# Optimization experiments

Measured on AMD Instinct MI355X. Metric: run time of the kernel, lower is better.

The kernel has to match this reference:

```python
import jax, jax.numpy as jnp
import numpy as np

N_NODES = 50000
N_EDGES = 640000
F = 128          # feat_dims == hidden_dims == out_channels
L = 5            # num_layers of GatedGraphConv


def setup_inputs() -> dict:
    key = jax.random.key(0)
    ks = jax.random.split(key, 9)
    s = 1.0 / np.sqrt(F)
    x = jax.random.normal(ks[0], (N_NODES, F), dtype=jnp.float32)
    edge_index = jax.random.randint(ks[1], (2, N_EDGES), 0, N_NODES, dtype=jnp.int64)
    weight = jax.random.uniform(ks[2], (L, F, F), jnp.float32, -s, s)   # per-layer linear
    w_ih = jax.random.uniform(ks[3], (3 * F, F), jnp.float32, -s, s)     # GRUCell input weights
    w_hh = jax.random.uniform(ks[4], (3 * F, F), jnp.float32, -s, s)     # GRUCell hidden weights
    b_ih = jax.random.uniform(ks[5], (3 * F,), jnp.float32, -s, s)
    b_hh = jax.random.uniform(ks[6], (3 * F,), jnp.float32, -s, s)
    lin_w = jax.random.uniform(ks[7], (1, F), jnp.float32, -s, s)
    lin_b = jax.random.uniform(ks[8], (1,), jnp.float32, -s, s)
    return {"x": x, "edge_index": edge_index, "weight": weight,
            "w_ih": w_ih, "w_hh": w_hh, "b_ih": b_ih, "b_hh": b_hh,
            "lin_w": lin_w, "lin_b": lin_b}


def _gru_cell(m, h, w_ih, w_hh, b_ih, b_hh):
    gi = m @ w_ih.T + b_ih          # [N, 3F]
    gh = h @ w_hh.T + b_hh          # [N, 3F]
    i_r, i_z, i_n = jnp.split(gi, 3, axis=-1)
    h_r, h_z, h_n = jnp.split(gh, 3, axis=-1)
    r = jax.nn.sigmoid(i_r + h_r)
    z = jax.nn.sigmoid(i_z + h_z)
    n = jnp.tanh(i_n + r * h_n)
    return (1.0 - z) * n + z * h


def reference(x, edge_index, weight, w_ih, w_hh, b_ih, b_hh, lin_w, lin_b):
    src = edge_index[0]   # message source (x_j)
    dst = edge_index[1]   # aggregation target
    n_nodes = x.shape[0]
    h = x  # in_channels == out_channels, no padding needed
    for i in range(L):
        m = h @ weight[i]                                   # [N, F]
        agg = jax.ops.segment_sum(m[src], dst, num_segments=n_nodes)  # add-aggregate
        h = _gru_cell(agg, h, w_ih, w_hh, b_ih, b_hh)
    out = jax.nn.relu(h) @ lin_w.T + lin_b                  # [N, 1]
    return out
```

## Files before the change

kernel.cpp:

```cpp
#include <hip/hip_runtime.h>

typedef float f32x4 __attribute__((ext_vector_type(4)));
typedef __bf16 bf16x8 __attribute__((ext_vector_type(8)));
typedef unsigned short u16x8 __attribute__((ext_vector_type(8)));

#define F 128

__device__ __forceinline__ unsigned short bf16_rne(float f) {
  unsigned u = __float_as_uint(f);
  u += 0x7FFFu + ((u >> 16) & 1u);
  return (unsigned short)(u >> 16);
}
__device__ __forceinline__ float bf16f(unsigned short s) {
  return __uint_as_float((unsigned)s << 16);
}


__global__ void split8_kernel(const float* __restrict__ in,
                              unsigned short* __restrict__ hi, unsigned short* __restrict__ lo,
                              int N) {
  int i = blockIdx.x * 256 + threadIdx.x;
  if (i >= N * 16) return;
  int node = i >> 4, f8 = i & 15;
  const float4* p = (const float4*)(in + (size_t)node * F + f8 * 8);
  float4 a = p[0], b = p[1];
  float v[8] = {a.x, a.y, a.z, a.w, b.x, b.y, b.z, b.w};
  u16x8 vh, vl;
#pragma unroll
  for (int e = 0; e < 8; ++e) {
    unsigned short x = bf16_rne(v[e]);
    vh[e] = x;
    vl[e] = bf16_rne(v[e] - bf16f(x));
  }
  size_t o = (size_t)node * F + f8 * 8;
  *(u16x8*)(hi + o) = vh;
  *(u16x8*)(lo + o) = vl;
}

__global__ void prep_w_kernel(const float* __restrict__ W, const float* __restrict__ w_ih,
                              const float* __restrict__ w_hh,
                              unsigned short* __restrict__ Bpack, int L) {
  int idx = blockIdx.x * 256 + threadIdx.x;
  if (idx >= L * 98304) return;
  int e = idx & 7;
  int l = (idx >> 3) & 63;
  int fp = idx >> 9;
  int part = fp % 3;
  int rest = fp / 3;
  int w = rest & 7, g = (rest >> 3) & 1, ks = (rest >> 4) & 3, t = rest >> 6;
  int j = part * 128 + w * 16 + (l & 15);
  int k = ks * 32 + ((l >> 4) & 3) * 8 + e;
  float v;
  if (g == 0) {
    const float* wi = w_ih + (size_t)j * 128;
    const float* wk = W + (size_t)t * 16384 + (size_t)k * 128;
    float acc = 0.f;
#pragma unroll 4
    for (int c = 0; c < 128; ++c) acc = fmaf(wk[c], wi[c], acc);
    v = acc;
  } else {
    v = w_hh[(size_t)j * 128 + k];
  }
  int ff = ((ks * 2 + g) * 8 + w) * 3 + part;
  size_t base = (size_t)t * 196608 + (size_t)ff * 1024 + l * 8 + e;
  unsigned short x = bf16_rne(v);
  Bpack[base] = x;
  Bpack[base + 512] = bf16_rne(v - bf16f(x));
}

__global__ void hist_kernel(const int* __restrict__ ei, int* __restrict__ cnt, int E) {
  int e = blockIdx.x * 256 + threadIdx.x;
  if (e < E) atomicAdd(&cnt[ei[E + e]], 1);
}

__global__ void scan1_kernel(const int* __restrict__ cnt, int* __restrict__ exscan,
                             int* __restrict__ chunk_sums, int N) {
  __shared__ int tmp[256];
  int i = blockIdx.x * 256 + threadIdx.x;
  int v = (i < N) ? cnt[i] : 0;
  tmp[threadIdx.x] = v;
  __syncthreads();
#pragma unroll
  for (int off = 1; off < 256; off <<= 1) {
    int a = (threadIdx.x >= off) ? tmp[threadIdx.x - off] : 0;
    __syncthreads();
    tmp[threadIdx.x] += a;
    __syncthreads();
  }
  if (i < N) exscan[i] = tmp[threadIdx.x] - v;
  if (threadIdx.x == 255) chunk_sums[blockIdx.x] = tmp[255];
}

__global__ void scan2_kernel(int* __restrict__ chunk_sums, int nchunk) {
  __shared__ int tmp[256];
  int v = (threadIdx.x < nchunk) ? chunk_sums[threadIdx.x] : 0;
  tmp[threadIdx.x] = v;
  __syncthreads();
#pragma unroll
  for (int off = 1; off < 256; off <<= 1) {
    int a = (threadIdx.x >= off) ? tmp[threadIdx.x - off] : 0;
    __syncthreads();
    tmp[threadIdx.x] += a;
    __syncthreads();
  }
  if (threadIdx.x < nchunk) chunk_sums[threadIdx.x] = tmp[threadIdx.x] - v;
}

__global__ void finalize_rowptr_kernel(const int* __restrict__ exscan,
                                       const int* __restrict__ chunk_sums,
                                       int* __restrict__ rowptr, int* __restrict__ cursor,
                                       int N, int E) {
  int i = blockIdx.x * 256 + threadIdx.x;
  if (i < N) {
    int v = exscan[i] + chunk_sums[i >> 8];
    rowptr[i] = v;
    cursor[i] = v;
  }
  if (i == N) rowptr[N] = E;
}

__global__ void place_kernel(const int* __restrict__ ei, int* __restrict__ cursor,
                             int* __restrict__ csr_src, int E) {
  int e = blockIdx.x * 256 + threadIdx.x;
  if (e >= E) return;
  int pos = atomicAdd(&cursor[ei[E + e]], 1);
  csr_src[pos] = ei[e];
}

__global__ __launch_bounds__(256) void gather_kernel(
    const unsigned short* __restrict__ hh, const unsigned short* __restrict__ hl,
    const int* __restrict__ rowptr, const int* __restrict__ csr_src,
    unsigned short* __restrict__ shi, unsigned short* __restrict__ slo, int N) {
  int node = blockIdx.x * 4 + (threadIdx.x >> 6);
  if (node >= N) return;
  const int lane = threadIdx.x & 63;
  const int grp = lane >> 4, sub = lane & 15;
  const int par = grp >> 1;
  const unsigned short* base = (grp & 1) ? hl : hh;
  const int beg = rowptr[node], end = rowptr[node + 1];
  float a[8] = {0.f, 0.f, 0.f, 0.f, 0.f, 0.f, 0.f, 0.f};
  int j = beg;
  for (; j + 8 <= end; j += 8) {
    int e0 = csr_src[j + par];
    int e1 = csr_src[j + 2 + par];
    int e2 = csr_src[j + 4 + par];
    int e3 = csr_src[j + 6 + par];
    u16x8 v0 = *(const u16x8*)(base + (size_t)e0 * F + sub * 8);
    u16x8 v1 = *(const u16x8*)(base + (size_t)e1 * F + sub * 8);
    u16x8 v2 = *(const u16x8*)(base + (size_t)e2 * F + sub * 8);
    u16x8 v3 = *(const u16x8*)(base + (size_t)e3 * F + sub * 8);
#pragma unroll
    for (int q = 0; q < 8; ++q)
      a[q] += (bf16f(v0[q]) + bf16f(v1[q])) + (bf16f(v2[q]) + bf16f(v3[q]));
  }
  for (; j + 2 <= end; j += 2) {
    int e0 = csr_src[j + par];
    u16x8 v0 = *(const u16x8*)(base + (size_t)e0 * F + sub * 8);
#pragma unroll
    for (int q = 0; q < 8; ++q) a[q] += bf16f(v0[q]);
  }
  if (j < end && par == 0) {
    int e0 = csr_src[j];
    u16x8 v0 = *(const u16x8*)(base + (size_t)e0 * F + sub * 8);
#pragma unroll
    for (int q = 0; q < 8; ++q) a[q] += bf16f(v0[q]);
  }
#pragma unroll
  for (int q = 0; q < 8; ++q) {
    a[q] += __shfl_xor(a[q], 32, 64);
    a[q] += __shfl_xor(a[q], 16, 64);
  }
  if (grp == 0) {
    u16x8 o;
#pragma unroll
    for (int q = 0; q < 8; ++q) o[q] = bf16_rne(a[q]);
    *(u16x8*)(shi + (size_t)node * F + sub * 8) = o;
  } else if (grp == 1) {
    u16x8 o;
#pragma unroll
    for (int q = 0; q < 8; ++q) {
      unsigned short x = bf16_rne(a[q]);
      o[q] = bf16_rne(a[q] - bf16f(x));
    }
    *(u16x8*)(slo + (size_t)node * F + sub * 8) = o;
  }
}

__device__ __forceinline__ void g2l(const void* g, void* l) {
  __builtin_amdgcn_global_load_lds((const __attribute__((address_space(1))) void*)g,
                                   (__attribute__((address_space(3))) void*)l, 16, 0, 0);
}

#define LOADB(hs, slot)                                                          \
  {                                                                              \
    const unsigned char* bg = Bbase + (size_t)(hs) * 49152;                      \
    _Pragma("unroll") for (int i = 0; i < 6; ++i)                                \
        Bf[slot][i] = *(const bf16x8*)(bg + i * 1024);                           \
  }
#define LOADA(hs, slot)                                                          \
  {                                                                              \
    const int ks_ = (hs) >> 1, g_ = (hs) & 1;                                    \
    const unsigned char* bh = lds + ((g_ * 2) * 4 + ks_) * 4096 + lrow * 64 + kq * 16;      \
    const unsigned char* bl = lds + ((g_ * 2 + 1) * 4 + ks_) * 4096 + lrow * 64 + kq * 16;  \
    _Pragma("unroll") for (int t = 0; t < 4; ++t) {                              \
      Af[slot][t] = *(const bf16x8*)(bh + t * 1024);                             \
      Af[slot][4 + t] = *(const bf16x8*)(bl + t * 1024);                         \
    }                                                                            \
  }
#define DOMFMA(hs, bslot, aslot)                                                 \
  {                                                                              \
    const int g_ = (hs) & 1;                                                     \
    __builtin_amdgcn_s_setprio(1);                                               \
    _Pragma("unroll") for (int part = 0; part < 3; ++part)                       \
        _Pragma("unroll") for (int t = 0; t < 4; ++t) {                          \
      const int ai = (part == 2) ? (t * 4 + 2 + g_) : (t * 4 + part);            \
      acc[ai] = __builtin_amdgcn_mfma_f32_16x16x32_bf16(Af[aslot][t], Bf[bslot][part * 2], acc[ai], 0, 0, 0);     \
      acc[ai] = __builtin_amdgcn_mfma_f32_16x16x32_bf16(Af[aslot][4 + t], Bf[bslot][part * 2], acc[ai], 0, 0, 0); \
      acc[ai] = __builtin_amdgcn_mfma_f32_16x16x32_bf16(Af[aslot][t], Bf[bslot][part * 2 + 1], acc[ai], 0, 0, 0); \
    }                                                                            \
    __builtin_amdgcn_s_setprio(0);                                               \
  }

#define ABSTRIDE 1056

__global__ __launch_bounds__(512, 2) void gemm_gru_kernel(
    const unsigned short* __restrict__ s_hi, const unsigned short* __restrict__ s_lo,
    const unsigned short* h_hi, const unsigned short* h_lo,
    const unsigned short* __restrict__ Bpack,
    const float* __restrict__ bih, const float* __restrict__ bhh,
    unsigned short* h_hi_out, unsigned short* h_lo_out, int N) {
  __shared__ __align__(1024) unsigned char lds[64 * ABSTRIDE];
  const int tid = threadIdx.x, w = tid >> 6, lane = tid & 63;
  const int lrow = lane & 15, kq = lane >> 4;
  const int row0 = blockIdx.x * 64;

  {
    const int arr = w >> 1;
    const unsigned short* ap = (arr == 0) ? s_hi : (arr == 1) ? s_lo : (arr == 2) ? h_hi : h_lo;
#pragma unroll
    for (int i = 0; i < 8; ++i) {
      const int ks = (2 * w + (i >> 2)) & 3;
      int r = row0 + (i & 3) * 16 + (lane >> 2);
      if (r >= N) r = N - 1;
      const unsigned short* g = ap + (size_t)r * F + ks * 32 + (lane & 3) * 8;
      g2l(g, lds + (w * 8 + i) * 1024 + lane * 16);
    }
  }

  f32x4 acc[16];
#pragma unroll
  for (int i = 0; i < 16; ++i) acc[i] = (f32x4){0.f, 0.f, 0.f, 0.f};
  bf16x8 Bf[3][6];
  bf16x8 Af[2][8];

  const unsigned char* Bbase = (const unsigned char*)Bpack + (size_t)w * 6144 + lane * 16;

  asm volatile("s_waitcnt vmcnt(0)" ::: "memory");
  __syncthreads();

  LOADB(0, 0) LOADA(0, 0) LOADB(1, 1) LOADB(2, 2)
  LOADA(1, 1) DOMFMA(0, 0, 0)
  LOADB(3, 0) LOADA(2, 0) DOMFMA(1, 1, 1)
  LOADB(4, 1) LOADA(3, 1) DOMFMA(2, 2, 0)
  LOADB(5, 2) LOADA(4, 0) DOMFMA(3, 0, 1)
  LOADB(6, 0) LOADA(5, 1) DOMFMA(4, 1, 0)
  LOADB(7, 1) LOADA(6, 0) DOMFMA(5, 2, 1)
  LOADA(7, 1) DOMFMA(6, 0, 0)
  DOMFMA(7, 1, 1)

  __syncthreads();

  const int row2 = tid >> 3, seg2 = tid & 7;
  const int r2 = row0 + row2;
  const size_t go2 = (size_t)(r2 < N ? r2 : 0) * F + seg2 * 16;
  u16x8 vh0 = *(const u16x8*)(h_hi_out + go2);
  u16x8 vh1 = *(const u16x8*)(h_hi_out + go2 + 8);
  u16x8 vl0 = *(const u16x8*)(h_lo_out + go2);
  u16x8 vl1 = *(const u16x8*)(h_lo_out + go2 + 8);

  {
    const int c = w * 16 + lrow;
    const float br = bih[c] + bhh[c];
    const float bz = bih[128 + c] + bhh[128 + c];
    const float bni = bih[256 + c], bnh = bhh[256 + c];
    unsigned char* abp = lds + (size_t)(kq * 4) * ABSTRIDE + c * 8;
#pragma unroll
    for (int t = 0; t < 4; ++t) {
#pragma unroll
      for (int i = 0; i < 4; ++i) {
        const float cr = acc[t * 4 + 0][i];
        const float cz = acc[t * 4 + 1][i];
        const float c1n = acc[t * 4 + 2][i], c2n = acc[t * 4 + 3][i];
        const float rr = 1.f / (1.f + __expf(-(cr + br)));
        const float zz = 1.f / (1.f + __expf(-(cz + bz)));
        const float nn = tanhf(c1n + bni + rr * (c2n + bnh));
        *(float2*)(abp + (size_t)(t * 16 + i) * ABSTRIDE) = make_float2((1.f - zz) * nn, zz);
      }
    }
  }
  __syncthreads();

  if (r2 < N) {
    const unsigned char* abp = lds + (size_t)row2 * ABSTRIDE + seg2 * 128;
    f32x4 p[8];
#pragma unroll
    for (int k = 0; k < 8; ++k) p[k] = *(const f32x4*)(abp + k * 16);
    u16x8 oh0, oh1, ol0, ol1;
#pragma unroll
    for (int k = 0; k < 4; ++k) {
      float h0 = bf16f(vh0[2 * k]) + bf16f(vl0[2 * k]);
      float h1 = bf16f(vh0[2 * k + 1]) + bf16f(vl0[2 * k + 1]);
      float n0 = p[k].x + p[k].y * h0;
      float n1 = p[k].z + p[k].w * h1;
      unsigned short x0 = bf16_rne(n0), x1 = bf16_rne(n1);
      oh0[2 * k] = x0;
      ol0[2 * k] = bf16_rne(n0 - bf16f(x0));
      oh0[2 * k + 1] = x1;
      ol0[2 * k + 1] = bf16_rne(n1 - bf16f(x1));
    }
#pragma unroll
    for (int k = 0; k < 4; ++k) {
      float h0 = bf16f(vh1[2 * k]) + bf16f(vl1[2 * k]);
      float h1 = bf16f(vh1[2 * k + 1]) + bf16f(vl1[2 * k + 1]);
      float n0 = p[4 + k].x + p[4 + k].y * h0;
      float n1 = p[4 + k].z + p[4 + k].w * h1;
      unsigned short x0 = bf16_rne(n0), x1 = bf16_rne(n1);
      oh1[2 * k] = x0;
      ol1[2 * k] = bf16_rne(n0 - bf16f(x0));
      oh1[2 * k + 1] = x1;
      ol1[2 * k + 1] = bf16_rne(n1 - bf16f(x1));
    }
    *(u16x8*)(h_hi_out + go2) = oh0;
    *(u16x8*)(h_hi_out + go2 + 8) = oh1;
    *(u16x8*)(h_lo_out + go2) = ol0;
    *(u16x8*)(h_lo_out + go2 + 8) = ol1;
  }
}

__global__ void final_kernel(const unsigned* __restrict__ hh, const unsigned* __restrict__ hl,
                             const float* __restrict__ lin_w,
                             const float* __restrict__ lin_b, float* __restrict__ out, int N) {
  int n = blockIdx.x * 4 + (threadIdx.x >> 6);
  if (n >= N) return;
  int d = threadIdx.x & 63;
  size_t o = (size_t)n * 64 + d;
  unsigned wh = hh[o], wl = hl[o];
  float v0 = bf16f((unsigned short)(wh & 0xffff)) + bf16f((unsigned short)(wl & 0xffff));
  float v1 = bf16f((unsigned short)(wh >> 16)) + bf16f((unsigned short)(wl >> 16));
  float sum = fmaxf(v0, 0.f) * lin_w[2 * d] + fmaxf(v1, 0.f) * lin_w[2 * d + 1];
#pragma unroll
  for (int s = 32; s; s >>= 1) sum += __shfl_xor(sum, s, 64);
  if (d == 0) out[n] = sum + lin_b[0];
}

extern "C" void kernel_launch(void* const* d_in, const int* in_sizes, int n_in,
                              void* d_out, int out_size, void* d_ws, size_t ws_size,
                              hipStream_t stream) {
  const float* x     = (const float*)d_in[0];
  const int*   ei    = (const int*)d_in[1];
  const float* W     = (const float*)d_in[2];
  const float* w_ih  = (const float*)d_in[3];
  const float* w_hh  = (const float*)d_in[4];
  const float* b_ih  = (const float*)d_in[5];
  const float* b_hh  = (const float*)d_in[6];
  const float* lin_w = (const float*)d_in[7];
  const float* lin_b = (const float*)d_in[8];

  const int N = in_sizes[0] / F;
  const int E = in_sizes[1] / 2;
  const int L = in_sizes[2] / (F * F);
  const size_t NF = (size_t)N * F;

  char* p = (char*)d_ws;
  unsigned short* h_hi = (unsigned short*)p; p += NF * 2;
  unsigned short* h_lo = (unsigned short*)p; p += NF * 2;
  unsigned short* s_hi = (unsigned short*)p; p += NF * 2;
  unsigned short* s_lo = (unsigned short*)p; p += NF * 2;
  unsigned short* Bpack = (unsigned short*)p; p += (size_t)L * 196608 * 2;
  int* cnt     = (int*)p; p += (size_t)N * 4;
  int* exscan  = (int*)p; p += (size_t)N * 4;
  int* chunk   = (int*)p; p += 256 * 4;
  int* rowptr  = (int*)p; p += ((size_t)N + 1) * 4;
  int* cursor  = (int*)p; p += (size_t)N * 4;
  int* csr_src = (int*)p; p += (size_t)E * 4;

  const int split_blocks = (N * 16 + 255) / 256;
  const int prep_blocks = (L * 98304 + 255) / 256;
  const int edge_blocks = (E + 255) / 256;
  const int nchunk = (N + 255) / 256;
  const int gemm_blocks = (N + 63) / 64;
  const int node4_blocks = (N + 3) / 4;

  split8_kernel<<<split_blocks, 256, 0, stream>>>(x, h_hi, h_lo, N);
  prep_w_kernel<<<prep_blocks, 256, 0, stream>>>(W, w_ih, w_hh, Bpack, L);

  hipMemsetAsync(cnt, 0, (size_t)N * 4, stream);
  hist_kernel<<<edge_blocks, 256, 0, stream>>>(ei, cnt, E);
  scan1_kernel<<<nchunk, 256, 0, stream>>>(cnt, exscan, chunk, N);
  scan2_kernel<<<1, 256, 0, stream>>>(chunk, nchunk);
  finalize_rowptr_kernel<<<(N + 256) / 256, 256, 0, stream>>>(exscan, chunk, rowptr, cursor, N, E);
  place_kernel<<<edge_blocks, 256, 0, stream>>>(ei, cursor, csr_src, E);

  for (int t = 0; t < L; ++t) {
    gather_kernel<<<node4_blocks, 256, 0, stream>>>(
        h_hi, h_lo, rowptr, csr_src, s_hi, s_lo, N);
    gemm_gru_kernel<<<gemm_blocks, 512, 0, stream>>>(
        s_hi, s_lo, h_hi, h_lo, Bpack + (size_t)t * 196608,
        b_ih, b_hh, h_hi, h_lo, N);
  }

  final_kernel<<<node4_blocks, 256, 0, stream>>>(
      (const unsigned*)h_hi, (const unsigned*)h_lo, lin_w, lin_b, (float*)d_out, N);
}
```

Baseline: 640.1 us.

## Fuse neighbor gather into GEMM-GRU kernel with ping-pong hidden buffers

Removes the separate gather kernel and has each GEMM-GRU block aggregate neighbor rows for its 64 nodes directly into LDS, skipping the global round-trip of the aggregated hi/lo arrays and one launch per layer. Hidden state now ping-pongs between two buffers so blocks can read previous-layer rows of other nodes while writing new ones. The cost is that the gather now runs at the GEMM kernel's occupancy (512 threads, 2 blocks per CU). Each 32-lane half processes one node at a time, which may expose gather latency and cause load imbalance from degree variance.

```diff
diff --git a/kernel.cpp b/kernel.cpp
--- a/kernel.cpp
+++ b/kernel.cpp
@@ -127,65 +127,6 @@
   csr_src[pos] = ei[e];
 }
 
-__global__ __launch_bounds__(256) void gather_kernel(
-    const unsigned short* __restrict__ hh, const unsigned short* __restrict__ hl,
-    const int* __restrict__ rowptr, const int* __restrict__ csr_src,
-    unsigned short* __restrict__ shi, unsigned short* __restrict__ slo, int N) {
-  int node = blockIdx.x * 4 + (threadIdx.x >> 6);
-  if (node >= N) return;
-  const int lane = threadIdx.x & 63;
-  const int grp = lane >> 4, sub = lane & 15;
-  const int par = grp >> 1;
-  const unsigned short* base = (grp & 1) ? hl : hh;
-  const int beg = rowptr[node], end = rowptr[node + 1];
-  float a[8] = {0.f, 0.f, 0.f, 0.f, 0.f, 0.f, 0.f, 0.f};
-  int j = beg;
-  for (; j + 8 <= end; j += 8) {
-    int e0 = csr_src[j + par];
-    int e1 = csr_src[j + 2 + par];
-    int e2 = csr_src[j + 4 + par];
-    int e3 = csr_src[j + 6 + par];
-    u16x8 v0 = *(const u16x8*)(base + (size_t)e0 * F + sub * 8);
-    u16x8 v1 = *(const u16x8*)(base + (size_t)e1 * F + sub * 8);
-    u16x8 v2 = *(const u16x8*)(base + (size_t)e2 * F + sub * 8);
-    u16x8 v3 = *(const u16x8*)(base + (size_t)e3 * F + sub * 8);
-#pragma unroll
-    for (int q = 0; q < 8; ++q)
-      a[q] += (bf16f(v0[q]) + bf16f(v1[q])) + (bf16f(v2[q]) + bf16f(v3[q]));
-  }
-  for (; j + 2 <= end; j += 2) {
-    int e0 = csr_src[j + par];
-    u16x8 v0 = *(const u16x8*)(base + (size_t)e0 * F + sub * 8);
-#pragma unroll
-    for (int q = 0; q < 8; ++q) a[q] += bf16f(v0[q]);
-  }
-  if (j < end && par == 0) {
-    int e0 = csr_src[j];
-    u16x8 v0 = *(const u16x8*)(base + (size_t)e0 * F + sub * 8);
-#pragma unroll
-    for (int q = 0; q < 8; ++q) a[q] += bf16f(v0[q]);
-  }
-#pragma unroll
-  for (int q = 0; q < 8; ++q) {
-    a[q] += __shfl_xor(a[q], 32, 64);
-    a[q] += __shfl_xor(a[q], 16, 64);
-  }
-  if (grp == 0) {
-    u16x8 o;
-#pragma unroll
-    for (int q = 0; q < 8; ++q) o[q] = bf16_rne(a[q]);
-    *(u16x8*)(shi + (size_t)node * F + sub * 8) = o;
-  } else if (grp == 1) {
-    u16x8 o;
-#pragma unroll
-    for (int q = 0; q < 8; ++q) {
-      unsigned short x = bf16_rne(a[q]);
-      o[q] = bf16_rne(a[q] - bf16f(x));
-    }
-    *(u16x8*)(slo + (size_t)node * F + sub * 8) = o;
-  }
-}
-
 __device__ __forceinline__ void g2l(const void* g, void* l) {
   __builtin_amdgcn_global_load_lds((const __attribute__((address_space(1))) void*)g,
                                    (__attribute__((address_space(3))) void*)l, 16, 0, 0);
@@ -223,20 +164,20 @@
 
 #define ABSTRIDE 1056
 
-__global__ __launch_bounds__(512, 2) void gemm_gru_kernel(
-    const unsigned short* __restrict__ s_hi, const unsigned short* __restrict__ s_lo,
-    const unsigned short* h_hi, const unsigned short* h_lo,
+__global__ __launch_bounds__(512, 2) void layer_kernel(
+    const unsigned short* __restrict__ hp_hi, const unsigned short* __restrict__ hp_lo,
+    unsigned short* __restrict__ hn_hi, unsigned short* __restrict__ hn_lo,
+    const int* __restrict__ rowptr, const int* __restrict__ csr_src,
     const unsigned short* __restrict__ Bpack,
-    const float* __restrict__ bih, const float* __restrict__ bhh,
-    unsigned short* h_hi_out, unsigned short* h_lo_out, int N) {
+    const float* __restrict__ bih, const float* __restrict__ bhh, int N) {
   __shared__ __align__(1024) unsigned char lds[64 * ABSTRIDE];
   const int tid = threadIdx.x, w = tid >> 6, lane = tid & 63;
   const int lrow = lane & 15, kq = lane >> 4;
   const int row0 = blockIdx.x * 64;
 
-  {
+  if (w >= 4) {
     const int arr = w >> 1;
-    const unsigned short* ap = (arr == 0) ? s_hi : (arr == 1) ? s_lo : (arr == 2) ? h_hi : h_lo;
+    const unsigned short* ap = (arr == 2) ? hp_hi : hp_lo;
 #pragma unroll
     for (int i = 0; i < 8; ++i) {
       const int ks = (2 * w + (i >> 2)) & 3;
@@ -244,6 +185,53 @@
       if (r >= N) r = N - 1;
       const unsigned short* g = ap + (size_t)r * F + ks * 32 + (lane & 3) * 8;
       g2l(g, lds + (w * 8 + i) * 1024 + lane * 16);
+    }
+  }
+
+  {
+    const int half = lane >> 5;
+    const int q = (lane >> 4) & 1;
+    const int fl = lane & 15;
+    const unsigned short* hb = (q ? hp_lo : hp_hi) + fl * 8;
+    unsigned char* sdst = lds + q * 16384 + (fl >> 2) * 4096 + (fl & 3) * 16;
+#pragma unroll 1
+    for (int pr = 0; pr < 4; ++pr) {
+      const int lr = w * 8 + pr * 2 + half;
+      int node = row0 + lr;
+      if (node >= N) node = N - 1;
+      int j = rowptr[node];
+      const int end = rowptr[node + 1];
+      float a[8] = {0.f, 0.f, 0.f, 0.f, 0.f, 0.f, 0.f, 0.f};
+      for (; j + 4 <= end; j += 4) {
+        int s0 = csr_src[j], s1 = csr_src[j + 1], s2 = csr_src[j + 2], s3 = csr_src[j + 3];
+        u16x8 v0 = *(const u16x8*)(hb + (size_t)s0 * F);
+        u16x8 v1 = *(const u16x8*)(hb + (size_t)s1 * F);
+        u16x8 v2 = *(const u16x8*)(hb + (size_t)s2 * F);
+        u16x8 v3 = *(const u16x8*)(hb + (size_t)s3 * F);
+#pragma unroll
+        for (int k = 0; k < 8; ++k)
+          a[k] += (bf16f(v0[k]) + bf16f(v1[k])) + (bf16f(v2[k]) + bf16f(v3[k]));
+      }
+      for (; j < end; ++j) {
+        int s0 = csr_src[j];
+        u16x8 v0 = *(const u16x8*)(hb + (size_t)s0 * F);
+#pragma unroll
+        for (int k = 0; k < 8; ++k) a[k] += bf16f(v0[k]);
+      }
+#pragma unroll
+      for (int k = 0; k < 8; ++k) a[k] += __shfl_xor(a[k], 16, 64);
+      u16x8 o;
+      if (q == 0) {
+#pragma unroll
+        for (int k = 0; k < 8; ++k) o[k] = bf16_rne(a[k]);
+      } else {
+#pragma unroll
+        for (int k = 0; k < 8; ++k) {
+          unsigned short x = bf16_rne(a[k]);
+          o[k] = bf16_rne(a[k] - bf16f(x));
+        }
+      }
+      *(u16x8*)(sdst + lr * 64) = o;
     }
   }
 
@@ -273,10 +261,10 @@
   const int row2 = tid >> 3, seg2 = tid & 7;
   const int r2 = row0 + row2;
   const size_t go2 = (size_t)(r2 < N ? r2 : 0) * F + seg2 * 16;
-  u16x8 vh0 = *(const u16x8*)(h_hi_out + go2);
-  u16x8 vh1 = *(const u16x8*)(h_hi_out + go2 + 8);
-  u16x8 vl0 = *(const u16x8*)(h_lo_out + go2);
-  u16x8 vl1 = *(const u16x8*)(h_lo_out + go2 + 8);
+  u16x8 vh0 = *(const u16x8*)(hp_hi + go2);
+  u16x8 vh1 = *(const u16x8*)(hp_hi + go2 + 8);
+  u16x8 vl0 = *(const u16x8*)(hp_lo + go2);
+  u16x8 vl1 = *(const u16x8*)(hp_lo + go2 + 8);
 
   {
     const int c = w * 16 + lrow;
@@ -330,10 +318,10 @@
       oh1[2 * k + 1] = x1;
       ol1[2 * k + 1] = bf16_rne(n1 - bf16f(x1));
     }
-    *(u16x8*)(h_hi_out + go2) = oh0;
-    *(u16x8*)(h_hi_out + go2 + 8) = oh1;
-    *(u16x8*)(h_lo_out + go2) = ol0;
-    *(u16x8*)(h_lo_out + go2 + 8) = ol1;
+    *(u16x8*)(hn_hi + go2) = oh0;
+    *(u16x8*)(hn_hi + go2 + 8) = oh1;
+    *(u16x8*)(hn_lo + go2) = ol0;
+    *(u16x8*)(hn_lo + go2 + 8) = ol1;
   }
 }
 
@@ -372,10 +360,10 @@
   const size_t NF = (size_t)N * F;
 
   char* p = (char*)d_ws;
-  unsigned short* h_hi = (unsigned short*)p; p += NF * 2;
-  unsigned short* h_lo = (unsigned short*)p; p += NF * 2;
-  unsigned short* s_hi = (unsigned short*)p; p += NF * 2;
-  unsigned short* s_lo = (unsigned short*)p; p += NF * 2;
+  unsigned short* hA_hi = (unsigned short*)p; p += NF * 2;
+  unsigned short* hA_lo = (unsigned short*)p; p += NF * 2;
+  unsigned short* hB_hi = (unsigned short*)p; p += NF * 2;
+  unsigned short* hB_lo = (unsigned short*)p; p += NF * 2;
   unsigned short* Bpack = (unsigned short*)p; p += (size_t)L * 196608 * 2;
   int* cnt     = (int*)p; p += (size_t)N * 4;
   int* exscan  = (int*)p; p += (size_t)N * 4;
@@ -388,10 +376,10 @@
   const int prep_blocks = (L * 98304 + 255) / 256;
   const int edge_blocks = (E + 255) / 256;
   const int nchunk = (N + 255) / 256;
-  const int gemm_blocks = (N + 63) / 64;
+  const int layer_blocks = (N + 63) / 64;
   const int node4_blocks = (N + 3) / 4;
 
-  split8_kernel<<<split_blocks, 256, 0, stream>>>(x, h_hi, h_lo, N);
+  split8_kernel<<<split_blocks, 256, 0, stream>>>(x, hA_hi, hA_lo, N);
   prep_w_kernel<<<prep_blocks, 256, 0, stream>>>(W, w_ih, w_hh, Bpack, L);
 
   hipMemsetAsync(cnt, 0, (size_t)N * 4, stream);
@@ -401,14 +389,15 @@
   finalize_rowptr_kernel<<<(N + 256) / 256, 256, 0, stream>>>(exscan, chunk, rowptr, cursor, N, E);
   place_kernel<<<edge_blocks, 256, 0, stream>>>(ei, cursor, csr_src, E);
 
+  unsigned short *cur_hi = hA_hi, *cur_lo = hA_lo, *nxt_hi = hB_hi, *nxt_lo = hB_lo;
   for (int t = 0; t < L; ++t) {
-    gather_kernel<<<node4_blocks, 256, 0, stream>>>(
-        h_hi, h_lo, rowptr, csr_src, s_hi, s_lo, N);
-    gemm_gru_kernel<<<gemm_blocks, 512, 0, stream>>>(
-        s_hi, s_lo, h_hi, h_lo, Bpack + (size_t)t * 196608,
-        b_ih, b_hh, h_hi, h_lo, N);
+    layer_kernel<<<layer_blocks, 512, 0, stream>>>(
+        cur_hi, cur_lo, nxt_hi, nxt_lo, rowptr, csr_src,
+        Bpack + (size_t)t * 196608, b_ih, b_hh, N);
+    unsigned short* th = cur_hi; cur_hi = nxt_hi; nxt_hi = th;
+    unsigned short* tl = cur_lo; cur_lo = nxt_lo; nxt_lo = tl;
   }
 
   final_kernel<<<node4_blocks, 256, 0, stream>>>(
-      (const unsigned*)h_hi, (const unsigned*)h_lo, lin_w, lin_b, (float*)d_out, N);
-}
+      (const unsigned*)cur_hi, (const unsigned*)cur_lo, lin_w, lin_b, (float*)d_out, N);
+}
```

Result: slower. 748.0 us (+16.8%).
